# Performance work log

Measured on AMD Instinct MI355X. Metric: run time of the kernel, lower is better.

## Reference

```python
import jax, jax.numpy as jnp
import numpy as np

B, C, H, W = 8, 256, 64, 64
HEADS, H_SP, W_SP = 8, 64, 4  # idx=0: H_sp=resolution[0], W_sp=split_size
D = C // HEADS
SCALE = D ** -0.5
HH, WW = H // H_SP, W // W_SP  # 1, 16 (no padding needed)


def setup_inputs() -> dict:
    key = jax.random.key(0)
    k1, k2, k3 = jax.random.split(key, 3)
    temp = jax.random.normal(k1, (B, 3, C, H, W), dtype=jnp.float32)
    get_v_weight = jax.random.normal(k2, (C, 1, 3, 3), dtype=jnp.float32) * 0.1
    get_v_bias = jax.random.normal(k3, (C,), dtype=jnp.float32) * 0.1
    return {"temp": temp, "get_v_weight": get_v_weight, "get_v_bias": get_v_bias}


def _im2win_shuffle(x):
    # x: (B, C, H, W); H split as (H_SP, HH) with H_SP OUTER (shuffled windows)
    x = x.reshape(B, HEADS, D, H_SP, HH, W_SP, WW)
    x = x.transpose(0, 4, 6, 1, 3, 5, 2)  # b hh ww h H_sp W_sp d
    return x.reshape(B * HH * WW, HEADS, H_SP * W_SP, D)


def reference(temp, get_v_weight, get_v_bias):
    # H, W are multiples of H_SP, W_SP -> pad is zero (faithful to F.pad path)
    q, k, v = temp[:, 0], temp[:, 1], temp[:, 2]
    qw = _im2win_shuffle(q) * SCALE
    kw = _im2win_shuffle(k)
    vw = _im2win_shuffle(v)

    # LePE: depthwise 3x3 conv applied per shuffled window
    vimg = v.reshape(B, C, H_SP, HH, W_SP, WW).transpose(0, 3, 5, 1, 2, 4)
    vimg = vimg.reshape(B * HH * WW, C, H_SP, W_SP)
    lepe = jax.lax.conv_general_dilated(
        vimg, get_v_weight, (1, 1), ((1, 1), (1, 1)),
        dimension_numbers=("NCHW", "OIHW", "NCHW"), feature_group_count=C,
    ) + get_v_bias[None, :, None, None]
    lepe = lepe.reshape(B * HH * WW, HEADS, D, H_SP * W_SP).transpose(0, 1, 3, 2)

    attn = jax.nn.softmax(jnp.einsum("whqd,whkd->whqk", qw, kw), axis=-1)
    x = jnp.einsum("whqk,whkd->whqd", attn, vw) + lepe  # (nW, h, S, d)

    # windows2img_shuffle -> (B, C, H, W), then raw .view to (B, H, W, C)
    x = x.reshape(B, HH, WW, HEADS, H_SP, W_SP, D)
    x = x.transpose(0, 3, 6, 4, 1, 5, 2).reshape(B, C, H, W)
    x = x.reshape(B, H, W, C)  # raw memory view, matches torch .view
    return x.reshape(B, H * W, C)
```

## Files before the change

kernel.cpp:

```cpp
#include <hip/hip_runtime.h>


typedef __attribute__((ext_vector_type(8))) short bf16x8;
typedef __attribute__((ext_vector_type(4))) float floatx4;
typedef unsigned short ushort_t;
typedef unsigned int uint_t;

constexpr float QSCALE = 0.25503486f;
constexpr size_t WS_NEED = 3ull * 1024 * 8192 * 2;

__device__ __forceinline__ ushort_t f2bf(float f) {
    union { float f; uint_t u; } v; v.f = f;
    uint_t r = v.u + 0x7fffu + ((v.u >> 16) & 1u);
    return (ushort_t)(r >> 16);
}
__device__ __forceinline__ float bf2f(ushort_t h) {
    union { uint_t u; float f; } v; v.u = ((uint_t)h) << 16;
    return v.f;
}

__global__ __launch_bounds__(256, 8)
void pack_kernel(const float* __restrict__ temp, ushort_t* __restrict__ ws)
{
    const int bi = blockIdx.x;
    const int b = bi / 384;
    const int rem = bi % 384;
    const int m = rem >> 7;
    const int hd = (rem >> 4) & 7;
    const int slab = rem & 15;

    __shared__ ushort_t Lb[4 * 2182];

    const int u = threadIdx.x;
    const float4* src4 = (const float4*)(temp + ((size_t)((b * 3 + m) * 256 + hd * 32)) * 4096);

    #pragma unroll
    for (int i = 0; i < 8; i++) {
        const int flat = i * 256 + u;
        const int w4 = flat & 15, h = (flat >> 4) & 3, d = flat >> 6;
        float4 v = src4[(size_t)d * 1024 + slab * 64 + h * 16 + w4];
        if (m == 0) { v.x *= QSCALE; v.y *= QSCALE; v.z *= QSCALE; v.w *= QSCALE; }
        const int base = h * 2182 + (w4 * 4) * 34 + d;
        Lb[base]       = f2bf(v.x);
        Lb[base + 34]  = f2bf(v.y);
        Lb[base + 68]  = f2bf(v.z);
        Lb[base + 102] = f2bf(v.w);
    }
    __syncthreads();

    const int t0 = slab * 16;
    if (m < 2) {
        #pragma unroll
        for (int i = 0; i < 4; i++) {
            const int c2 = i * 256 + u;
            const int dc = c2 & 3, tl = (c2 >> 2) & 15, ww = c2 >> 6;
            const int h = tl >> 2, w = (tl & 3) * 16 + ww;
            const uint_t* lp = (const uint_t*)&Lb[h * 2182 + w * 34 + dc * 8];
            uint4 val; val.x = lp[0]; val.y = lp[1]; val.z = lp[2]; val.w = lp[3];
            const size_t prob = (size_t)((b * 8 + hd) * 16 + ww);
            *(uint4*)(ws + prob * 16384 + (size_t)m * 8192 + (t0 + tl) * 32 + dc * 8) = val;
        }
    } else {
        #pragma unroll
        for (int i = 0; i < 2; i++) {
            const int c2 = i * 256 + u;
            const int d = c2 & 31, ww = (c2 >> 5) & 15;
            union { ushort_t us[16]; uint4 q[2]; } vv;
            #pragma unroll
            for (int tl = 0; tl < 16; tl++)
                vv.us[tl] = Lb[(tl >> 2) * 2182 + ((tl & 3) * 16 + ww) * 34 + d];
            const size_t prob = (size_t)((b * 8 + hd) * 16 + ww);
            uint4* dst = (uint4*)(ws + 16777216ull + prob * 8192 + d * 256 + t0);
            dst[0] = vv.q[0]; dst[1] = vv.q[1];
        }
    }
}

template<bool PACKED>
__global__ __launch_bounds__(256, 4)
void attn_kernel(const float* __restrict__ temp, ushort_t* __restrict__ ws,
                 const float* __restrict__ wgt, const float* __restrict__ bias,
                 float* __restrict__ out)
{
    const int B_ = blockIdx.x;
    const int bh = B_ & 63, ww = B_ >> 6;
    const int hd = bh & 7, b = bh >> 3;
    const int plin = bh * 16 + ww;

    __shared__ ushort_t Ks[256 * 40];
    __shared__ ushort_t Vt[32 * 264];

    const int u = threadIdx.x;
    const int wv = u >> 6, ln = u & 63;
    const int lm = ln & 15, q4 = ln >> 4, l7 = ln & 7, b8 = (ln >> 3) & 1;

    const int pa_w0 = (wv * 64 + b8 * 16 + q4 * 4) * 40 + 32 + l7;
    const int pa_w1 = (wv * 64 + (2 + b8) * 16 + q4 * 4) * 40 + 32 + l7;
    const int pa_rd = (wv * 64 + ln) * 40 + 32;

    bf16x8 qa[4];

    if (PACKED) {
        const size_t pb = (size_t)plin * 16384;
        {
            const uint4* s = (const uint4*)(ws + pb + 8192 + u * 32);
            uint4* d = (uint4*)&Ks[u * 40];
            d[0] = s[0]; d[1] = s[1]; d[2] = s[2]; d[3] = s[3];
        }
        {
            const int dd = u >> 3, seg = u & 7;
            const uint4* s = (const uint4*)(ws + 16777216ull + (size_t)plin * 8192 + dd * 256 + seg * 32);
            uint4* d = (uint4*)&Vt[dd * 264 + seg * 32];
            d[0] = s[0]; d[1] = s[1]; d[2] = s[2]; d[3] = s[3];
        }
        #pragma unroll
        for (int T = 0; T < 4; T++) {
            const int Tg = wv * 4 + T;
            qa[T] = *(const bf16x8*)(ws + pb + (Tg * 16 + lm) * 32 + q4 * 8);
        }
    } else {
        const float* qp = temp + ((size_t)(b * 3 + 0) * 256 + hd * 32) * 4096 + ww;
        const float* kp = temp + ((size_t)(b * 3 + 1) * 256 + hd * 32) * 4096 + ww;
        const float* vp = temp + ((size_t)(b * 3 + 2) * 256 + hd * 32) * 4096 + ww;
        {
            union { ushort_t us[32]; uint4 q[4]; } tmp;
            #pragma unroll
            for (int d = 0; d < 32; d++) tmp.us[d] = f2bf(kp[(size_t)d * 4096 + u * 16]);
            uint4* dst = (uint4*)&Ks[u * 40];
            dst[0] = tmp.q[0]; dst[1] = tmp.q[1]; dst[2] = tmp.q[2]; dst[3] = tmp.q[3];
        }
        #pragma unroll
        for (int d = 0; d < 32; d++) Vt[d * 264 + u] = f2bf(vp[(size_t)d * 4096 + u * 16]);
        #pragma unroll
        for (int T = 0; T < 4; T++) {
            const int Tg = wv * 4 + T, q = Tg * 16 + lm;
            union { ushort_t us[8]; bf16x8 v; } f;
            #pragma unroll
            for (int j = 0; j < 8; j++)
                f.us[j] = f2bf(qp[(size_t)(q4 * 8 + j) * 4096 + q * 16] * QSCALE);
            qa[T] = f.v;
        }
    }
    __syncthreads();

    floatx4 acc[4][2];
    float lrow[4][4];
    #pragma unroll
    for (int T = 0; T < 4; T++) {
        acc[T][0] = (floatx4)0.0f; acc[T][1] = (floatx4)0.0f;
        #pragma unroll
        for (int r = 0; r < 4; r++) lrow[T][r] = 0.0f;
    }

    for (int c = 0; c < 8; c++) {
        const bf16x8 kb0 = *(const bf16x8*)&Ks[(c * 32 + lm) * 40 + q4 * 8];
        const bf16x8 kb1 = *(const bf16x8*)&Ks[(c * 32 + 16 + lm) * 40 + q4 * 8];
        const bf16x8 vb0 = *(const bf16x8*)&Vt[lm * 264 + c * 32 + q4 * 8];
        const bf16x8 vb1 = *(const bf16x8*)&Vt[(16 + lm) * 264 + c * 32 + q4 * 8];
        #pragma unroll
        for (int T = 0; T < 4; T++) {
            floatx4 s0 = __builtin_amdgcn_mfma_f32_16x16x32_bf16(qa[T], kb0, (floatx4)0.0f, 0, 0, 0);
            floatx4 s1 = __builtin_amdgcn_mfma_f32_16x16x32_bf16(qa[T], kb1, (floatx4)0.0f, 0, 0, 0);
            #pragma unroll
            for (int r = 0; r < 4; r++) {
                const float p0 = exp2f(s0[r]);
                const float p1 = exp2f(s1[r]);
                const ushort_t h0 = f2bf(p0), h1 = f2bf(p1);
                lrow[T][r] += bf2f(h0) + bf2f(h1);
                Ks[pa_w0 + r * 40] = h0;
                Ks[pa_w1 + r * 40] = h1;
            }
            const bf16x8 pa = *(const bf16x8*)&Ks[pa_rd];
            acc[T][0] = __builtin_amdgcn_mfma_f32_16x16x32_bf16(pa, vb0, acc[T][0], 0, 0, 0);
            acc[T][1] = __builtin_amdgcn_mfma_f32_16x16x32_bf16(pa, vb1, acc[T][1], 0, 0, 0);
        }
    }

    float wc[2][9], bs[2];
    #pragma unroll
    for (int dt = 0; dt < 2; dt++) {
        const int d = dt * 16 + lm;
        #pragma unroll
        for (int k = 0; k < 9; k++) wc[dt][k] = wgt[(hd * 32 + d) * 9 + k];
        bs[dt] = bias[hd * 32 + d];
    }

    float* Of = (float*)ws + (size_t)plin * 8192;
    float* ob = out + ((size_t)b * 256 + hd * 32) * 4096 + ww;

    #pragma unroll
    for (int T = 0; T < 4; T++) {
        const int Tg = wv * 4 + T;
        const int hs = Tg * 4 + q4;
        float inv[4];
        #pragma unroll
        for (int r = 0; r < 4; r++) {
            float ls = lrow[T][r];
            ls += __shfl_xor(ls, 1); ls += __shfl_xor(ls, 2);
            ls += __shfl_xor(ls, 4); ls += __shfl_xor(ls, 8);
            inv[r] = 1.0f / ls;
        }
        #pragma unroll
        for (int dt = 0; dt < 2; dt++) {
            const int d = dt * 16 + lm;
            float vv[3][4];
            #pragma unroll
            for (int dy = 0; dy < 3; dy++) {
                const int hh = hs + dy - 1;
                if (hh >= 0 && hh < 64) {
                    #pragma unroll
                    for (int cx = 0; cx < 4; cx++) vv[dy][cx] = bf2f(Vt[d * 264 + hh * 4 + cx]);
                } else {
                    #pragma unroll
                    for (int cx = 0; cx < 4; cx++) vv[dy][cx] = 0.0f;
                }
            }
            #pragma unroll
            for (int r = 0; r < 4; r++) {
                float lep = bs[dt];
                #pragma unroll
                for (int dy = 0; dy < 3; dy++) {
                    #pragma unroll
                    for (int kx = 0; kx < 3; kx++) {
                        const int wsrc = r + kx - 1;
                        if (wsrc >= 0 && wsrc < 4) lep += wc[dt][dy * 3 + kx] * vv[dy][wsrc];
                    }
                }
                const int q = Tg * 16 + q4 * 4 + r;
                const float val = acc[T][dt][r] * inv[r] + lep;
                if (PACKED) Of[q * 32 + d] = val;
                else        ob[(size_t)d * 4096 + q * 16] = val;
            }
        }
    }
}

__global__ __launch_bounds__(256, 4)
void scatter_kernel(const float* __restrict__ Of, float* __restrict__ out)
{
    const int bi = blockIdx.x;
    const int b = bi >> 7, hd = (bi >> 4) & 7, slab = bi & 15;
    const int bh = b * 8 + hd;
    const int t0 = slab * 16;

    __shared__ float T2[16 * 545];

    const int u = threadIdx.x;

    #pragma unroll
    for (int i = 0; i < 8; i++) {
        const int f = i * 256 + u;
        const int d4 = f & 7, t = (f >> 3) & 15, ww = f >> 7;
        const float4 v = ((const float4*)Of)[(size_t)(bh * 16 + ww) * 2048 + (t0 + t) * 8 + d4];
        const int base = t * 545 + (d4 * 4) * 17 + ww;
        T2[base]      = v.x;
        T2[base + 17] = v.y;
        T2[base + 34] = v.z;
        T2[base + 51] = v.w;
    }
    __syncthreads();

    float4* out4 = (float4*)(out + ((size_t)b * 256 + hd * 32) * 4096);
    #pragma unroll
    for (int i = 0; i < 8; i++) {
        const int g = i * 256 + u;
        const int ww4 = g & 3, t = (g >> 2) & 15, d = g >> 6;
        const int base = t * 545 + d * 17 + ww4 * 4;
        float4 v;
        v.x = T2[base]; v.y = T2[base + 1]; v.z = T2[base + 2]; v.w = T2[base + 3];
        out4[(size_t)d * 1024 + (t0 + t) * 4 + ww4] = v;
    }
}

extern "C" void kernel_launch(void* const* d_in, const int* in_sizes, int n_in,
                              void* d_out, int out_size, void* d_ws, size_t ws_size,
                              hipStream_t stream) {
    const float* temp = (const float*)d_in[0];
    const float* wgt  = (const float*)d_in[1];
    const float* bias = (const float*)d_in[2];
    float* out = (float*)d_out;

    if (ws_size >= WS_NEED) {
        ushort_t* ws = (ushort_t*)d_ws;
        pack_kernel<<<dim3(3072), dim3(256), 0, stream>>>(temp, ws);
        attn_kernel<true><<<dim3(1024), dim3(256), 0, stream>>>(temp, ws, wgt, bias, out);
        scatter_kernel<<<dim3(1024), dim3(256), 0, stream>>>((const float*)d_ws, out);
    } else {
        attn_kernel<false><<<dim3(1024), dim3(256), 0, stream>>>(temp, (ushort_t*)d_ws, wgt, bias, out);
    }
}
```

Before: 213.7 us.

## Split K/V staging into two halves overlapped with compute; store intermediate output as bf16

The attention kernel now loads only the first half of K and V into shared memory before compute starts. The second half is held in registers, computed over chunks 0-3, then written to shared memory behind a barrier before chunks 4-7. The intermediate output written to the workspace and read by the scatter kernel switches from fp32 to bf16, which halves that round-trip traffic. This adds rounding error to the final output and costs extra registers and a second barrier.

```diff
diff --git a/kernel.cpp b/kernel.cpp
--- a/kernel.cpp
+++ b/kernel.cpp
@@ -99,24 +99,25 @@
     const int pa_rd = (wv * 64 + ln) * 40 + 32;
 
     bf16x8 qa[4];
+    const int krow = u >> 1, khalf = u & 1;
+    const int vdd = u >> 3, vseg = u & 7;
 
     if (PACKED) {
         const size_t pb = (size_t)plin * 16384;
-        {
-            const uint4* s = (const uint4*)(ws + pb + 8192 + u * 32);
-            uint4* d = (uint4*)&Ks[u * 40];
-            d[0] = s[0]; d[1] = s[1]; d[2] = s[2]; d[3] = s[3];
-        }
-        {
-            const int dd = u >> 3, seg = u & 7;
-            const uint4* s = (const uint4*)(ws + 16777216ull + (size_t)plin * 8192 + dd * 256 + seg * 32);
-            uint4* d = (uint4*)&Vt[dd * 264 + seg * 32];
-            d[0] = s[0]; d[1] = s[1]; d[2] = s[2]; d[3] = s[3];
-        }
+        const ushort_t* gK = ws + pb + 8192;
+        const ushort_t* gV = ws + 16777216ull + (size_t)plin * 8192;
         #pragma unroll
         for (int T = 0; T < 4; T++) {
             const int Tg = wv * 4 + T;
             qa[T] = *(const bf16x8*)(ws + pb + (Tg * 16 + lm) * 32 + q4 * 8);
+        }
+        {
+            const uint4* s = (const uint4*)(gK + krow * 32 + khalf * 16);
+            uint4* d = (uint4*)&Ks[krow * 40 + khalf * 16];
+            d[0] = s[0]; d[1] = s[1];
+            const uint4* sv = (const uint4*)(gV + vdd * 256 + vseg * 16);
+            uint4* dv = (uint4*)&Vt[vdd * 264 + vseg * 16];
+            dv[0] = sv[0]; dv[1] = sv[1];
         }
     } else {
         const float* qp = temp + ((size_t)(b * 3 + 0) * 256 + hd * 32) * 4096 + ww;
@@ -152,7 +153,18 @@
         for (int r = 0; r < 4; r++) lrow[T][r] = 0.0f;
     }
 
-    for (int c = 0; c < 8; c++) {
+    uint4 kB0, kB1, vB0, vB1;
+    if (PACKED) {
+        const size_t pb = (size_t)plin * 16384;
+        const ushort_t* gK = ws + pb + 8192;
+        const ushort_t* gV = ws + 16777216ull + (size_t)plin * 8192;
+        const uint4* s = (const uint4*)(gK + (128 + krow) * 32 + khalf * 16);
+        kB0 = s[0]; kB1 = s[1];
+        const uint4* sv = (const uint4*)(gV + vdd * 256 + 128 + vseg * 16);
+        vB0 = sv[0]; vB1 = sv[1];
+    }
+
+    auto chunk = [&](int c) {
         const bf16x8 kb0 = *(const bf16x8*)&Ks[(c * 32 + lm) * 40 + q4 * 8];
         const bf16x8 kb1 = *(const bf16x8*)&Ks[(c * 32 + 16 + lm) * 40 + q4 * 8];
         const bf16x8 vb0 = *(const bf16x8*)&Vt[lm * 264 + c * 32 + q4 * 8];
@@ -174,6 +186,22 @@
             acc[T][0] = __builtin_amdgcn_mfma_f32_16x16x32_bf16(pa, vb0, acc[T][0], 0, 0, 0);
             acc[T][1] = __builtin_amdgcn_mfma_f32_16x16x32_bf16(pa, vb1, acc[T][1], 0, 0, 0);
         }
+    };
+
+    if (PACKED) {
+        #pragma unroll
+        for (int c = 0; c < 4; c++) chunk(c);
+        {
+            uint4* d = (uint4*)&Ks[(128 + krow) * 40 + khalf * 16];
+            d[0] = kB0; d[1] = kB1;
+            uint4* dv = (uint4*)&Vt[vdd * 264 + 128 + vseg * 16];
+            dv[0] = vB0; dv[1] = vB1;
+        }
+        __syncthreads();
+        #pragma unroll
+        for (int c = 4; c < 8; c++) chunk(c);
+    } else {
+        for (int c = 0; c < 8; c++) chunk(c);
     }
 
     float wc[2][9], bs[2];
@@ -185,7 +213,7 @@
         bs[dt] = bias[hd * 32 + d];
     }
 
-    float* Of = (float*)ws + (size_t)plin * 8192;
+    ushort_t* Of = ws + (size_t)plin * 16384;
     float* ob = out + ((size_t)b * 256 + hd * 32) * 4096 + ww;
 
     #pragma unroll
@@ -228,7 +256,7 @@
                 }
                 const int q = Tg * 16 + q4 * 4 + r;
                 const float val = acc[T][dt][r] * inv[r] + lep;
-                if (PACKED) Of[q * 32 + d] = val;
+                if (PACKED) Of[q * 32 + d] = f2bf(val);
                 else        ob[(size_t)d * 4096 + q * 16] = val;
             }
         }
@@ -236,7 +264,7 @@
 }
 
 __global__ __launch_bounds__(256, 4)
-void scatter_kernel(const float* __restrict__ Of, float* __restrict__ out)
+void scatter_kernel(const ushort_t* __restrict__ Of, float* __restrict__ out)
 {
     const int bi = blockIdx.x;
     const int b = bi >> 7, hd = (bi >> 4) & 7, slab = bi & 15;
@@ -248,15 +276,15 @@
     const int u = threadIdx.x;
 
     #pragma unroll
-    for (int i = 0; i < 8; i++) {
+    for (int i = 0; i < 4; i++) {
         const int f = i * 256 + u;
-        const int d4 = f & 7, t = (f >> 3) & 15, ww = f >> 7;
-        const float4 v = ((const float4*)Of)[(size_t)(bh * 16 + ww) * 2048 + (t0 + t) * 8 + d4];
-        const int base = t * 545 + (d4 * 4) * 17 + ww;
-        T2[base]      = v.x;
-        T2[base + 17] = v.y;
-        T2[base + 34] = v.z;
-        T2[base + 51] = v.w;
+        const int d4 = f & 3, t = (f >> 2) & 15, ww = f >> 6;
+        const ushort_t* s = Of + (size_t)(bh * 16 + ww) * 16384 + (t0 + t) * 32 + d4 * 8;
+        union { uint4 q; ushort_t us[8]; } v;
+        v.q = *(const uint4*)s;
+        const int base = t * 545 + (d4 * 8) * 17 + ww;
+        #pragma unroll
+        for (int j = 0; j < 8; j++) T2[base + j * 17] = bf2f(v.us[j]);
     }
     __syncthreads();
 
@@ -284,7 +312,7 @@
         ushort_t* ws = (ushort_t*)d_ws;
         pack_kernel<<<dim3(3072), dim3(256), 0, stream>>>(temp, ws);
         attn_kernel<true><<<dim3(1024), dim3(256), 0, stream>>>(temp, ws, wgt, bias, out);
-        scatter_kernel<<<dim3(1024), dim3(256), 0, stream>>>((const float*)d_ws, out);
+        scatter_kernel<<<dim3(1024), dim3(256), 0, stream>>>((const ushort_t*)d_ws, out);
     } else {
         attn_kernel<false><<<dim3(1024), dim3(256), 0, stream>>>(temp, (ushort_t*)d_ws, wgt, bias, out);
     }
```

New measurement: 262.7 us. 22.9% more time.
